# Optimization experiments

Hardware: AMD Instinct MI355X
Metric: run time of the kernel (lower is better)

Reference implementation:

```python
import jax, jax.numpy as jnp
import numpy as np

B, S, T = 32, 128, 64
V, E, H = 32000, 256, 512


def setup_inputs() -> dict:
    key = jax.random.key(0)
    ks = jax.random.split(key, 32)
    n = jax.random.normal

    def lin(k, fi, fo):
        kw, kb = jax.random.split(k)
        s = 1.0 / np.sqrt(fi)
        return (jax.random.uniform(kw, (fi, fo), jnp.float32, -s, s),
                jax.random.uniform(kb, (fo,), jnp.float32, -s, s))

    W_enc, b_enc = lin(ks[4], 2 * H, H)      # attention.enc_h_in
    W_prev, b_prev = lin(ks[5], H, H)        # attention.prev_s_in
    W_att, b_att = lin(ks[6], H, 1)          # attention.linear
    Wi_g, bi_g = lin(ks[7], E, 2 * H)        # cell.input_weights
    Wh_g, bh_g = lin(ks[8], H, 2 * H)        # cell.hidden_weights
    Wc_g, bc_g = lin(ks[9], 2 * H, 2 * H)    # cell.ctx_weights
    Wi, bi = lin(ks[10], E, H)               # cell.input_in
    Wh, bh = lin(ks[11], H, H)               # cell.hidden_in
    Wc, bc = lin(ks[12], 2 * H, H)           # cell.ctx_in
    W_out, b_out = lin(ks[13], H, V)         # dec2word

    return dict(
        content=n(ks[0], (B, H), jnp.float32),
        sentiment=n(ks[1], (B, H), jnp.float32),
        hiddens=n(ks[2], (B, S, 2 * H), jnp.float32),
        target=jax.random.randint(ks[3], (B, T), 0, V, jnp.int32),
        embed=n(ks[14], (V, E), jnp.float32) * 0.02,
        W_enc=W_enc, b_enc=b_enc, W_prev=W_prev, b_prev=b_prev,
        W_att=W_att, b_att=b_att,
        Wi_g=Wi_g, bi_g=bi_g, Wh_g=Wh_g, bh_g=bh_g, Wc_g=Wc_g, bc_g=bc_g,
        Wi=Wi, bi=bi, Wh=Wh, bh=bh, Wc=Wc, bc=bc,
        W_out=W_out, b_out=b_out,
    )


def reference(content, sentiment, hiddens, target, embed,
              W_enc, b_enc, W_prev, b_prev, W_att, b_att,
              Wi_g, bi_g, Wh_g, bh_g, Wc_g, bc_g,
              Wi, bi, Wh, bh, Wc, bc, W_out, b_out):
    tgt_emb = embed[target]                       # [B, T, E]
    enc_proj = hiddens @ W_enc + b_enc            # [B, S, H], timestep-invariant

    def step(prev_s, x_t):
        # additive attention
        q = prev_s @ W_prev + b_prev              # [B, H]
        h = jnp.tanh(enc_proj + q[:, None, :])    # [B, S, H]
        score = h @ W_att + b_att                 # [B, S, 1]
        alpha = jax.nn.softmax(score, axis=1)     # over source positions
        ctx = jnp.einsum('bsi,bsh->bh', alpha, hiddens)  # [B, 2H]
        # GRU-like cell (original uses only the first gate, as written)
        gates = x_t @ Wi_g + bi_g + prev_s @ Wh_g + bh_g + ctx @ Wc_g + bc_g
        reset_gate, _update_gate = jnp.split(gates, 2, axis=1)
        r = jax.nn.sigmoid(reset_gate)
        s_tilde = jnp.tanh(x_t @ Wi + bi + prev_s @ Wh + bh + ctx @ Wc + bc)
        new_s = (1.0 - r) * prev_s + r * s_tilde
        return new_s, new_s

    _, dec_h = jax.lax.scan(step, content, jnp.swapaxes(tgt_emb, 0, 1))
    dec_h = jnp.swapaxes(dec_h, 0, 1)             # [B, T, H]
    style_logits = sentiment @ W_out + b_out      # [B, V], same every step
    outputs = (dec_h @ W_out + b_out) + 0.5 * style_logits[:, None, :]
    return outputs                                # [B, T, V]
```

## Files before the change

### kernel.cpp

```cpp
#include <hip/hip_runtime.h>
#include <hip/hip_bf16.h>
#include <math.h>

#define NB 32
#define NS 128
#define NT 64
#define NV 32000
#define NE 256
#define NH 512

typedef short s16x8 __attribute__((ext_vector_type(8)));
typedef float f32x4 __attribute__((ext_vector_type(4)));
typedef unsigned u32x4 __attribute__((ext_vector_type(4)));

__device__ __forceinline__ unsigned short f2bf(float x) {
    union { float f; unsigned u; } v; v.f = x;
    unsigned r = v.u + 0x7FFFu + ((v.u >> 16) & 1u);
    return (unsigned short)(r >> 16);
}
__device__ __forceinline__ float bf2f(short h) {
    union { unsigned u; float f; } x;
    x.u = ((unsigned)(unsigned short)h) << 16;
    return x.f;
}

__device__ __forceinline__ void bar_lgkm() {
    asm volatile("s_waitcnt lgkmcnt(0)" ::: "memory");
    __builtin_amdgcn_sched_barrier(0);
    __builtin_amdgcn_s_barrier();
    __builtin_amdgcn_sched_barrier(0);
}

__device__ __forceinline__ void st_pt(unsigned long long* p, unsigned pay, unsigned tag) {
    unsigned long long v = (unsigned long long)pay | ((unsigned long long)tag << 32);
    asm volatile("global_store_dwordx2 %0, %1, off sc0 sc1" :: "v"(p), "v"(v) : "memory");
}
__device__ __forceinline__ void st_coh32(unsigned* p, unsigned v) {
    asm volatile("global_store_dword %0, %1, off sc0 sc1" :: "v"(p), "v"(v) : "memory");
}
__device__ __forceinline__ unsigned ld_coh32(const unsigned* p) {
    unsigned v;
    asm volatile("global_load_dword %0, %1, off sc0 sc1\n\ts_waitcnt vmcnt(0)"
                 : "=v"(v) : "v"(p) : "memory");
    return v;
}
__device__ __forceinline__ u32x4 ld_coh_x4(const void* p) {
    u32x4 v;
    asm volatile("global_load_dwordx4 %0, %1, off sc0 sc1\n\ts_waitcnt vmcnt(0)"
                 : "=&v"(v) : "v"(p) : "memory");
    return v;
}
__device__ __forceinline__ void ld8_pt(const unsigned long long* b0, unsigned long long* v) {
    unsigned long long v0, v1, v2, v3, v4, v5, v6, v7;
    asm volatile(
        "global_load_dwordx2 %0, %8, off sc0 sc1\n\t"
        "global_load_dwordx2 %1, %9, off sc0 sc1\n\t"
        "global_load_dwordx2 %2, %10, off sc0 sc1\n\t"
        "global_load_dwordx2 %3, %11, off sc0 sc1\n\t"
        "global_load_dwordx2 %4, %12, off sc0 sc1\n\t"
        "global_load_dwordx2 %5, %13, off sc0 sc1\n\t"
        "global_load_dwordx2 %6, %14, off sc0 sc1\n\t"
        "global_load_dwordx2 %7, %15, off sc0 sc1\n\t"
        "s_waitcnt vmcnt(0)"
        : "=&v"(v0), "=&v"(v1), "=&v"(v2), "=&v"(v3),
          "=&v"(v4), "=&v"(v5), "=&v"(v6), "=&v"(v7)
        : "v"(b0), "v"(b0 + 1024), "v"(b0 + 2048), "v"(b0 + 3072),
          "v"(b0 + 4096), "v"(b0 + 5120), "v"(b0 + 6144), "v"(b0 + 7168)
        : "memory");
    v[0] = v0; v[1] = v1; v[2] = v2; v[3] = v3;
    v[4] = v4; v[5] = v5; v[6] = v6; v[7] = v7;
}
__device__ __forceinline__ void ld3_pt(const unsigned long long* p0,
                                       const unsigned long long* p1,
                                       const unsigned long long* p2,
                                       unsigned long long& a, unsigned long long& b,
                                       unsigned long long& c) {
    asm volatile(
        "global_load_dwordx2 %0, %3, off sc0 sc1\n\t"
        "global_load_dwordx2 %1, %4, off sc0 sc1\n\t"
        "global_load_dwordx2 %2, %5, off sc0 sc1\n\t"
        "s_waitcnt vmcnt(0)"
        : "=&v"(a), "=&v"(b), "=&v"(c)
        : "v"(p0), "v"(p1), "v"(p2)
        : "memory");
}

__global__ void build_wfrag_k(const float* __restrict__ Wp,
                              const float* __restrict__ Whg,
                              const float* __restrict__ Wh,
                              unsigned short* __restrict__ wfrag) {
    int blk = blockIdx.x;
    int lane = threadIdx.x;
    int ct = blk >> 4, kt = blk & 15;
    int c = ct * 16 + (lane & 15);
    int kb = kt * 32 + (lane >> 4) * 8;
    s16x8 v;
#pragma unroll
    for (int j = 0; j < 8; ++j) {
        int k = kb + j;
        float x;
        if (c < 512)       x = Wp[k * 512 + c];
        else if (c < 1024) x = Whg[k * 1024 + (c - 512)];
        else               x = Wh[k * 512 + (c - 1024)];
        v[j] = (short)f2bf(x);
    }
    ((s16x8*)wfrag)[blk * 64 + lane] = v;
}

template<int MODE>
__global__ __launch_bounds__(256, 2) void gemm_mfma(
    const float* __restrict__ Af, const unsigned short* __restrict__ Abf,
    const int* __restrict__ gidx,
    const float* __restrict__ B0, const float* __restrict__ B1, const float* __restrict__ B2,
    const float* __restrict__ e0, const float* __restrict__ e1, const float* __restrict__ e2,
    const float* __restrict__ e3, const float* __restrict__ e4, const float* __restrict__ e5,
    void* __restrict__ O0v, void* __restrict__ O1v, void* __restrict__ O2v)
{
    constexpr int M   = (MODE == 0) ? 4096 : 2048;
    constexpr int K   = (MODE == 0) ? 1024 : 256;
    constexpr int LDA = (MODE == 0) ? 1024 : 256;
    constexpr int MB  = M / 128;

    const int bm = blockIdx.x % MB, bn = blockIdx.x / MB;
    const int m0 = bm * 128, n0 = bn * 128;

    const float* Bp; int ldb, coff;
    if constexpr (MODE == 0) {
        int sub = n0 >> 9;
        Bp   = (sub == 0) ? B0 : (sub == 1) ? B1 : B2;
        ldb  = (sub == 1) ? 1024 : 512;
        coff = n0 & 511;
    } else {
        if (n0 < 512) { Bp = B0; ldb = 1024; coff = n0; }
        else          { Bp = B1; ldb = 512;  coff = n0 - 512; }
    }

    __shared__ unsigned short As[128 * 40];
    __shared__ unsigned short Bs[128 * 40];

    const int tid = threadIdx.x, lane = tid & 63, w = tid >> 6;
    const int wr = w >> 1, wc = w & 1;
    const int k0f = (lane >> 4) * 8;
    const int rsel = lane & 15;

    f32x4 acc[4][4];
#pragma unroll
    for (int i = 0; i < 4; ++i)
#pragma unroll
        for (int j = 0; j < 4; ++j) { f32x4 z = {0.f, 0.f, 0.f, 0.f}; acc[i][j] = z; }

    for (int kt = 0; kt < K / 32; ++kt) {
        const int k0 = kt * 32;
        __syncthreads();
#pragma unroll
        for (int i = 0; i < 16; ++i) {
            int idx = tid + i * 256;
            int r = idx >> 5, k = idx & 31;
            unsigned short v;
            if constexpr (MODE == 1) {
                int g = gidx[m0 + r];
                v = f2bf(Af[(size_t)g * 256 + k0 + k]);
            } else {
                v = f2bf(Af[(size_t)(m0 + r) * LDA + k0 + k]);
            }
            As[r * 40 + k] = v;
        }
#pragma unroll
        for (int i = 0; i < 16; ++i) {
            int idx = tid + i * 256;
            int k = idx >> 7, c = idx & 127;
            Bs[c * 40 + k] = f2bf(Bp[(size_t)(k0 + k) * ldb + coff + c]);
        }
        __syncthreads();

        s16x8 af[4], bf[4];
#pragma unroll
        for (int i = 0; i < 4; ++i)
            af[i] = *(const s16x8*)&As[(wr * 64 + i * 16 + rsel) * 40 + k0f];
#pragma unroll
        for (int j = 0; j < 4; ++j)
            bf[j] = *(const s16x8*)&Bs[(wc * 64 + j * 16 + rsel) * 40 + k0f];
#pragma unroll
        for (int i = 0; i < 4; ++i)
#pragma unroll
            for (int j = 0; j < 4; ++j)
                acc[i][j] = __builtin_amdgcn_mfma_f32_16x16x32_bf16(af[i], bf[j], acc[i][j], 0, 0, 0);
    }

    const int rg = (lane >> 4) * 4;
#pragma unroll
    for (int i = 0; i < 4; ++i)
#pragma unroll
        for (int j = 0; j < 4; ++j) {
            int row0 = m0 + wr * 64 + i * 16 + rg;
            int col  = n0 + wc * 64 + j * 16 + rsel;
            if constexpr (MODE == 0) {
                int sub = col >> 9;
                if (sub == 0) {
                    unsigned short* Ta = (unsigned short*)O0v;
#pragma unroll
                    for (int r = 0; r < 4; ++r)
                        Ta[(size_t)(row0 + r) * 512 + col] = f2bf(tanhf(acc[i][j][r] + e0[col]));
                } else {
                    int h = col & 511;
                    int bb = row0 >> 7, s0 = row0 & 127;
                    unsigned long long pk = 0;
#pragma unroll
                    for (int r = 0; r < 4; ++r)
                        pk |= (unsigned long long)f2bf(acc[i][j][r]) << (16 * r);
                    unsigned short* dstp = (sub == 1) ? (unsigned short*)O1v : (unsigned short*)O2v;
                    *(unsigned long long*)&dstp[(size_t)((bb * 512 + h) * 128 + s0)] = pk;
                }
            } else {
                float* Of = (float*)O0v;
                float bias;
                if (col < 512) bias = e0[col] + e1[col] + e2[col];
                else { int h = col - 512; bias = e3[h] + e4[h] + e5[h]; }
#pragma unroll
                for (int r = 0; r < 4; ++r)
                    Of[(size_t)(row0 + r) * 1024 + col] = acc[i][j][r] + bias;
            }
        }
}

__global__ __launch_bounds__(1024) void fused_scan_out(
    const float* __restrict__ content, const float* __restrict__ sentiment,
    const float* __restrict__ b_prev,  const float* __restrict__ W_att,
    const unsigned short* __restrict__ Ta_bf,
    const unsigned short* __restrict__ hWcg_t,
    const unsigned short* __restrict__ hWc_t,
    const float* __restrict__ xgxs, const unsigned short* __restrict__ wfrag,
    unsigned long long* __restrict__ Spl, unsigned long long* __restrict__ Upl,
    unsigned short* __restrict__ dh, unsigned* __restrict__ prog,
    const float* __restrict__ W_out, const float* __restrict__ b_out,
    float* __restrict__ out)
{
    __shared__ __attribute__((aligned(16))) char smem[90624];
    const int tid = threadIdx.x, lane = tid & 63, w = tid >> 6;

    if (blockIdx.x < NB) {
        const int b = blockIdx.x;
        unsigned short* W_lds = (unsigned short*)smem;
        unsigned short* S_lds = (unsigned short*)(smem + 49152);
        float* tq = (float*)(smem + 83456);
        float* sc = (float*)(smem + 85504);
        float* al = (float*)(smem + 86016);
        float* cg = (float*)(smem + 86528);
        float* cs = (float*)(smem + 88576);

        {
            const s16x8* src = (const s16x8*)wfrag + (size_t)b * (3 * 16 * 64);
            s16x8* dst = (s16x8*)W_lds;
            for (int i = tid; i < 3 * 16 * 64; i += 1024) dst[i] = src[i];
        }
        float s_reg = 0.f, senth = 0.f, bprev_h = 0.f;
        if (tid < 512) {
            s_reg   = content[b * 512 + tid];
            senth   = 0.5f * sentiment[b * 512 + tid];
            bprev_h = b_prev[tid];
        }
        float wv[8];
        {
            const f32x4* wa = (const f32x4*)&W_att[lane * 8];
            f32x4 a0 = wa[0], a1 = wa[1];
#pragma unroll
            for (int j = 0; j < 4; ++j) { wv[j] = a0[j]; wv[4 + j] = a1[j]; }
        }
        const int kbase = (lane >> 4) * 8;
        const int mat = tid >> 9, hh = tid & 511;
        const s16x8* Mp = (const s16x8*)((mat ? hWc_t : hWcg_t) + ((size_t)(b * 512 + hh)) * 128);

        if (tid < 512) {
            float nsn = __shfl_down(s_reg, 1, 64);
            if (!(lane & 1)) {
                unsigned pay = (unsigned)f2bf(s_reg) | ((unsigned)f2bf(nsn) << 16);
                st_pt(&Spl[b * 256 + (tid >> 1)], pay, 1u);
            }
        }

        for (int t = 0; t < 64; ++t) {
            const unsigned want = (unsigned)(t + 1);
            float xg_pre = 0.f, xs_pre = 0.f;
            if (tid < 512) {
                xg_pre = xgxs[((size_t)b * 64 + t) * 1024 + tid];
                xs_pre = xgxs[((size_t)b * 64 + t) * 1024 + 512 + tid];
            }

            {
                unsigned long long v[8];
                const unsigned long long* base = &Spl[tid];
                ld8_pt(base, v);
                for (;;) {
                    bool ok = true;
#pragma unroll
                    for (int ii = 0; ii < 8; ++ii) ok &= ((unsigned)(v[ii] >> 32) == want);
                    if (ok) break;
                    __builtin_amdgcn_s_sleep(1);
                    ld8_pt(base, v);
                }
#pragma unroll
                for (int ii = 0; ii < 8; ++ii) {
                    int idx = tid + ii * 1024;
                    int r = idx >> 8, c = (idx & 255) * 2;
                    *(unsigned*)&S_lds[r * 536 + c] = (unsigned)v[ii];
                }
            }
            bar_lgkm();

            if (w < 6) {
                const int mt = w & 1, ct = w >> 1;
                const int arow = mt * 16 + (lane & 15);
                f32x4 ae = {0.f, 0.f, 0.f, 0.f}, ao = {0.f, 0.f, 0.f, 0.f};
                const s16x8* wl = (const s16x8*)W_lds;
#pragma unroll
                for (int kt = 0; kt < 16; kt += 2) {
                    s16x8 a0 = *(const s16x8*)&S_lds[arow * 536 + kt * 32 + kbase];
                    s16x8 a1 = *(const s16x8*)&S_lds[arow * 536 + (kt + 1) * 32 + kbase];
                    ae = __builtin_amdgcn_mfma_f32_16x16x32_bf16(a0, wl[(ct * 16 + kt) * 64 + lane], ae, 0, 0, 0);
                    ao = __builtin_amdgcn_mfma_f32_16x16x32_bf16(a1, wl[(ct * 16 + kt + 1) * 64 + lane], ao, 0, 0, 0);
                }
                f32x4 a4 = ae + ao;
                const int cout = b * 48 + ct * 16 + (lane & 15);
                const int rbase = mt * 16 + (lane >> 4) * 4;
#pragma unroll
                for (int r = 0; r < 4; ++r)
                    st_pt(&Upl[(size_t)(rbase + r) * 1536 + cout], __float_as_uint(a4[r]), want);
            }

            float guv = 0.f, suv = 0.f;
            if (tid < 512) {
                unsigned long long u0, u1, u2;
                const unsigned long long* q0 = &Upl[b * 1536 + tid];
                const unsigned long long* q1 = &Upl[b * 1536 + 512 + tid];
                const unsigned long long* q2 = &Upl[b * 1536 + 1024 + tid];
                ld3_pt(q0, q1, q2, u0, u1, u2);
                while (((unsigned)(u0 >> 32) != want) | ((unsigned)(u1 >> 32) != want) |
                       ((unsigned)(u2 >> 32) != want)) {
                    __builtin_amdgcn_s_sleep(1);
                    ld3_pt(q0, q1, q2, u0, u1, u2);
                }
                float qv = __uint_as_float((unsigned)u0);
                guv = __uint_as_float((unsigned)u1);
                suv = __uint_as_float((unsigned)u2);
                tq[tid] = tanhf(qv + bprev_h);
            }
            bar_lgkm();

            {
                float tqv[8];
                const f32x4* tp = (const f32x4*)&tq[lane * 8];
                f32x4 t0 = tp[0], t1 = tp[1];
#pragma unroll
                for (int j = 0; j < 4; ++j) { tqv[j] = t0[j]; tqv[4 + j] = t1[j]; }
#pragma unroll
                for (int s8 = 0; s8 < 8; ++s8) {
                    int s = w * 8 + s8;
                    s16x8 tv = *(const s16x8*)&Ta_bf[((size_t)(b * 128 + s)) * 512 + lane * 8];
                    float a = 0.f;
#pragma unroll
                    for (int j = 0; j < 8; ++j) {
                        float ta = bf2f(tv[j]);
                        float num = ta + tqv[j];
                        float den = fmaf(ta, tqv[j], 1.0f);
                        a = fmaf(wv[j], num * __builtin_amdgcn_rcpf(den), a);
                    }
#pragma unroll
                    for (int off = 32; off; off >>= 1) a += __shfl_xor(a, off, 64);
                    if (lane == 0) sc[s] = a;
                }
            }
            bar_lgkm();
            if (w == 0) {
                float v0 = sc[lane], v1 = sc[lane + 64];
                float m = fmaxf(v0, v1);
#pragma unroll
                for (int off = 32; off; off >>= 1) m = fmaxf(m, __shfl_xor(m, off, 64));
                float p0 = __expf(v0 - m), p1 = __expf(v1 - m);
                float sm = p0 + p1;
#pragma unroll
                for (int off = 32; off; off >>= 1) sm += __shfl_xor(sm, off, 64);
                float inv = __builtin_amdgcn_rcpf(sm);
                al[lane] = p0 * inv; al[lane + 64] = p1 * inv;
            }
            bar_lgkm();
            {
                float a0 = 0.f, a1 = 0.f;
#pragma unroll
                for (int q = 0; q < 16; ++q) {
                    s16x8 v = Mp[q];
#pragma unroll
                    for (int j = 0; j < 8; j += 2) {
                        a0 = fmaf(al[q * 8 + j],     bf2f(v[j]),     a0);
                        a1 = fmaf(al[q * 8 + j + 1], bf2f(v[j + 1]), a1);
                    }
                }
                if (mat) cs[hh] = a0 + a1; else cg[hh] = a0 + a1;
            }
            bar_lgkm();
            if (tid < 512) {
                int h = tid;
                float g  = guv + xg_pre + cg[h];
                float r  = __builtin_amdgcn_rcpf(1.0f + __expf(-g));
                float sp = suv + xs_pre + cs[h];
                float e  = __expf(2.0f * sp);
                float st = 1.0f - 2.0f * __builtin_amdgcn_rcpf(e + 1.0f);
                float ns = s_reg + r * (st - s_reg);
                s_reg = ns;
                float dv = ns + senth;
                float dvn = __shfl_down(dv, 1, 64);
                if (!(lane & 1)) {
                    unsigned pk = (unsigned)f2bf(dv) | ((unsigned)f2bf(dvn) << 16);
                    st_coh32((unsigned*)dh + ((((size_t)t * 32 + b) * 512 + h) >> 1), pk);
                }
                if (t < 63) {
                    float nsn = __shfl_down(ns, 1, 64);
                    if (!(lane & 1)) {
                        unsigned pay = (unsigned)f2bf(ns) | ((unsigned)f2bf(nsn) << 16);
                        st_pt(&Spl[b * 256 + (h >> 1)], pay, (unsigned)(t + 2));
                    }
                }
            }
            if ((t & 7) == 7) asm volatile("s_waitcnt vmcnt(0)" ::: "memory");
            bar_lgkm();
            if ((t & 7) == 7 && tid == 0)
                st_coh32(&prog[b * 16], (unsigned)(t + 1));
        }
    } else {
        unsigned short* As = (unsigned short*)smem;
        unsigned short* Bs = (unsigned short*)(smem + 20480);
        const int k4 = blockIdx.x - NB;
        const int wr = w >> 2, wc = w & 3;
        const int k0f = (lane >> 4) * 8;
        const int rsel = lane & 15;
        const int rg = (lane >> 4) * 4;
        const int ar = tid >> 2, akofs = (tid & 3) * 8;
        const int bk = tid >> 5, bc8 = (tid & 31) * 8;

        for (int idx = k4; idx < 1000; idx += 224) {
            const int tm = idx / 125, tn = idx - tm * 125;
            const unsigned need = (unsigned)(tm * 8 + 8);
            if (w == 0) {
                for (;;) {
                    unsigned v = 0xFFFFFFFFu;
                    if (lane < 32) v = ld_coh32(&prog[lane * 16]);
                    if (__all(v >= need)) break;
                    __builtin_amdgcn_s_sleep(32);
                }
            }
            __syncthreads();

            const int m0 = tm * 256, n0 = tn * 256;
            f32x4 acc[4][4];
#pragma unroll
            for (int i = 0; i < 4; ++i)
#pragma unroll
                for (int j = 0; j < 4; ++j) { f32x4 z = {0.f, 0.f, 0.f, 0.f}; acc[i][j] = z; }

            for (int kt = 0; kt < 16; ++kt) {
                const int k0 = kt * 32;
                __syncthreads();
                {
                    u32x4 a = ld_coh_x4(&dh[(size_t)(m0 + ar) * 512 + k0 + akofs]);
                    *(u32x4*)&As[ar * 40 + akofs] = a;
                }
                {
                    const float* bp = &W_out[(size_t)(k0 + bk) * 32000 + n0 + bc8];
#pragma unroll
                    for (int j = 0; j < 8; ++j) Bs[(bc8 + j) * 40 + bk] = f2bf(bp[j]);
                }
                __syncthreads();

                s16x8 af[4], bfr[4];
#pragma unroll
                for (int i = 0; i < 4; ++i)
                    af[i] = *(const s16x8*)&As[(wr * 64 + i * 16 + rsel) * 40 + k0f];
#pragma unroll
                for (int j = 0; j < 4; ++j)
                    bfr[j] = *(const s16x8*)&Bs[(wc * 64 + j * 16 + rsel) * 40 + k0f];
#pragma unroll
                for (int i = 0; i < 4; ++i)
#pragma unroll
                    for (int j = 0; j < 4; ++j)
                        acc[i][j] = __builtin_amdgcn_mfma_f32_16x16x32_bf16(af[i], bfr[j], acc[i][j], 0, 0, 0);
            }

#pragma unroll
            for (int i = 0; i < 4; ++i)
#pragma unroll
                for (int j = 0; j < 4; ++j) {
                    int trow0 = m0 + wr * 64 + i * 16 + rg;
                    int col   = n0 + wc * 64 + j * 16 + rsel;
                    float bb_ = 1.5f * b_out[col];
#pragma unroll
                    for (int r = 0; r < 4; ++r) {
                        int trow = trow0 + r;
                        int bb = trow & 31, tt = trow >> 5;
                        out[(size_t)(bb * 64 + tt) * 32000 + col] = acc[i][j][r] + bb_;
                    }
                }
        }
    }
}

extern "C" void kernel_launch(void* const* d_in, const int* in_sizes, int n_in,
                              void* d_out, int out_size, void* d_ws, size_t ws_size,
                              hipStream_t stream) {
    const float* content  = (const float*)d_in[0];
    const float* sentiment= (const float*)d_in[1];
    const float* hiddens  = (const float*)d_in[2];
    const int*   target   = (const int*)  d_in[3];
    const float* embed    = (const float*)d_in[4];
    const float* W_enc = (const float*)d_in[5];  const float* b_enc = (const float*)d_in[6];
    const float* W_prev= (const float*)d_in[7];  const float* b_prev= (const float*)d_in[8];
    const float* W_att = (const float*)d_in[9];
    const float* Wi_g  = (const float*)d_in[11]; const float* bi_g  = (const float*)d_in[12];
    const float* Wh_g  = (const float*)d_in[13]; const float* bh_g  = (const float*)d_in[14];
    const float* Wc_g  = (const float*)d_in[15]; const float* bc_g  = (const float*)d_in[16];
    const float* Wi    = (const float*)d_in[17]; const float* bi    = (const float*)d_in[18];
    const float* Wh    = (const float*)d_in[19]; const float* bh    = (const float*)d_in[20];
    const float* Wc    = (const float*)d_in[21]; const float* bc    = (const float*)d_in[22];
    const float* W_out = (const float*)d_in[23]; const float* b_out = (const float*)d_in[24];
    float* out = (float*)d_out;

    char* ws = (char*)d_ws;
    unsigned short* wfrag = (unsigned short*)ws;
    unsigned long long* Spl = (unsigned long long*)(ws + 0x180000);
    unsigned long long* Upl = (unsigned long long*)(ws + 0x190000);
    unsigned* prog = (unsigned*)(ws + 0x1F0000);
    unsigned short* Ta_bf   = (unsigned short*)(ws + 0x200000);
    unsigned short* hWcg_t  = (unsigned short*)(ws + 0x600000);
    unsigned short* hWc_t   = (unsigned short*)(ws + 0xA00000);
    float* xgxs     = (float*)(ws + 0xE00000);
    unsigned short* dh      = (unsigned short*)(ws + 0x1600000);

    hipMemsetAsync(ws + 0x180000, 0, 0x70800, stream);

    build_wfrag_k<<<96 * 16, 64, 0, stream>>>(W_prev, Wh_g, Wh, wfrag);

    gemm_mfma<0><<<32 * 12, 256, 0, stream>>>(
        hiddens, nullptr, nullptr, W_enc, Wc_g, Wc,
        b_enc, nullptr, nullptr, nullptr, nullptr, nullptr,
        (void*)Ta_bf, (void*)hWcg_t, (void*)hWc_t);

    gemm_mfma<1><<<16 * 8, 256, 0, stream>>>(
        embed, nullptr, target, Wi_g, Wi, nullptr,
        bi_g, bh_g, bc_g, bi, bh, bc,
        (void*)xgxs, nullptr, nullptr);

    fused_scan_out<<<256, 1024, 0, stream>>>(
        content, sentiment, b_prev, W_att, Ta_bf, hWcg_t, hWc_t,
        xgxs, wfrag, Spl, Upl, dh, prog, W_out, b_out, out);

    (void)in_sizes; (void)n_in; (void)out_size; (void)ws_size;
}
```

Measured before the change: 1.337 ms.

## Prepack W_out into MFMA-fragment bf16 layout before output GEMM

```diff
diff --git a/kernel.cpp b/kernel.cpp
--- a/kernel.cpp
+++ b/kernel.cpp
@@ -44,11 +44,18 @@
                  : "=v"(v) : "v"(p) : "memory");
     return v;
 }
-__device__ __forceinline__ u32x4 ld_coh_x4(const void* p) {
-    u32x4 v;
-    asm volatile("global_load_dwordx4 %0, %1, off sc0 sc1\n\ts_waitcnt vmcnt(0)"
-                 : "=&v"(v) : "v"(p) : "memory");
-    return v;
+__device__ __forceinline__ void st_coh_x4(void* p, u32x4 v) {
+    asm volatile("global_store_dwordx4 %0, %1, off sc0 sc1" :: "v"(p), "v"(v) : "memory");
+}
+__device__ __forceinline__ void ld64_coh(const void* p, u32x4& a, u32x4& b, u32x4& c, u32x4& d) {
+    asm volatile(
+        "global_load_dwordx4 %0, %4, off sc0 sc1\n\t"
+        "global_load_dwordx4 %1, %4, off offset:16 sc0 sc1\n\t"
+        "global_load_dwordx4 %2, %4, off offset:32 sc0 sc1\n\t"
+        "global_load_dwordx4 %3, %4, off offset:48 sc0 sc1\n\t"
+        "s_waitcnt vmcnt(0)"
+        : "=&v"(a), "=&v"(b), "=&v"(c), "=&v"(d)
+        : "v"(p) : "memory");
 }
 __device__ __forceinline__ void ld8_pt(const unsigned long long* b0, unsigned long long* v) {
     unsigned long long v0, v1, v2, v3, v4, v5, v6, v7;
@@ -232,6 +239,7 @@
     const float* __restrict__ xgxs, const unsigned short* __restrict__ wfrag,
     unsigned long long* __restrict__ Spl, unsigned long long* __restrict__ Upl,
     unsigned short* __restrict__ dh, unsigned* __restrict__ prog,
+    unsigned* __restrict__ packdone, unsigned short* __restrict__ wpk,
     const float* __restrict__ W_out, const float* __restrict__ b_out,
     float* __restrict__ out)
 {
@@ -426,15 +434,38 @@
                 st_coh32(&prog[b * 16], (unsigned)(t + 1));
         }
     } else {
+        const int k4 = blockIdx.x - NB;
         unsigned short* As = (unsigned short*)smem;
-        unsigned short* Bs = (unsigned short*)(smem + 20480);
-        const int k4 = blockIdx.x - NB;
+
+        for (int u = k4 * 16 + w; u < 32000; u += 224 * 16) {
+            int ct = u >> 4, kt = u & 15;
+            int c = ct * 16 + (lane & 15);
+            int kb = kt * 32 + (lane >> 4) * 8;
+            s16x8 v;
+#pragma unroll
+            for (int j = 0; j < 8; ++j)
+                v[j] = (short)f2bf(W_out[(size_t)(kb + j) * 32000 + c]);
+            union { s16x8 s; u32x4 u4; } cv; cv.s = v;
+            st_coh_x4(&wpk[(size_t)u * 512 + (size_t)lane * 8], cv.u4);
+        }
+        asm volatile("s_waitcnt vmcnt(0)" ::: "memory");
+        __syncthreads();
+        if (tid == 0)
+            __hip_atomic_fetch_add(packdone, 1u, __ATOMIC_RELAXED, __HIP_MEMORY_SCOPE_AGENT);
+        if (w == 0 && lane == 0) {
+            while (__hip_atomic_load(packdone, __ATOMIC_RELAXED, __HIP_MEMORY_SCOPE_AGENT) < 224u)
+                __builtin_amdgcn_s_sleep(16);
+        }
+        __syncthreads();
+        __builtin_amdgcn_fence(__ATOMIC_ACQUIRE, "agent");
+        __syncthreads();
+
         const int wr = w >> 2, wc = w & 3;
         const int k0f = (lane >> 4) * 8;
         const int rsel = lane & 15;
         const int rg = (lane >> 4) * 4;
-        const int ar = tid >> 2, akofs = (tid & 3) * 8;
-        const int bk = tid >> 5, bc8 = (tid & 31) * 8;
+        const int ar4 = tid >> 2, aq = tid & 3;
+        const s16x8* wpk8 = (const s16x8*)wpk;
 
         for (int idx = k4; idx < 1000; idx += 224) {
             const int tm = idx / 125, tn = idx - tm * 125;
@@ -456,32 +487,36 @@
 #pragma unroll
                 for (int j = 0; j < 4; ++j) { f32x4 z = {0.f, 0.f, 0.f, 0.f}; acc[i][j] = z; }
 
-            for (int kt = 0; kt < 16; ++kt) {
-                const int k0 = kt * 32;
+#pragma unroll
+            for (int kq = 0; kq < 4; ++kq) {
                 __syncthreads();
                 {
-                    u32x4 a = ld_coh_x4(&dh[(size_t)(m0 + ar) * 512 + k0 + akofs]);
-                    *(u32x4*)&As[ar * 40 + akofs] = a;
-                }
-                {
-                    const float* bp = &W_out[(size_t)(k0 + bk) * 32000 + n0 + bc8];
-#pragma unroll
-                    for (int j = 0; j < 8; ++j) Bs[(bc8 + j) * 40 + bk] = f2bf(bp[j]);
+                    const unsigned short* sp = &dh[(size_t)(m0 + ar4) * 512 + kq * 128 + aq * 32];
+                    u32x4 a0, a1, a2, a3;
+                    ld64_coh(sp, a0, a1, a2, a3);
+                    int base = ar4 * 136 + aq * 32;
+                    *(u32x4*)&As[base]      = a0;
+                    *(u32x4*)&As[base + 8]  = a1;
+                    *(u32x4*)&As[base + 16] = a2;
+                    *(u32x4*)&As[base + 24] = a3;
                 }
                 __syncthreads();
-
-                s16x8 af[4], bfr[4];
-#pragma unroll
-                for (int i = 0; i < 4; ++i)
-                    af[i] = *(const s16x8*)&As[(wr * 64 + i * 16 + rsel) * 40 + k0f];
-#pragma unroll
-                for (int j = 0; j < 4; ++j)
-                    bfr[j] = *(const s16x8*)&Bs[(wc * 64 + j * 16 + rsel) * 40 + k0f];
-#pragma unroll
-                for (int i = 0; i < 4; ++i)
+#pragma unroll
+                for (int kk = 0; kk < 4; ++kk) {
+                    const int kt = kq * 4 + kk;
+                    s16x8 bfr[4], af[4];
 #pragma unroll
                     for (int j = 0; j < 4; ++j)
-                        acc[i][j] = __builtin_amdgcn_mfma_f32_16x16x32_bf16(af[i], bfr[j], acc[i][j], 0, 0, 0);
+                        bfr[j] = wpk8[(size_t)(((tn * 16 + wc * 4 + j) * 16 + kt)) * 64 + lane];
+#pragma unroll
+                    for (int i = 0; i < 4; ++i)
+                        af[i] = *(const s16x8*)&As[(wr * 64 + i * 16 + rsel) * 136 + kk * 32 + k0f];
+#pragma unroll
+                    for (int i = 0; i < 4; ++i)
+#pragma unroll
+                        for (int j = 0; j < 4; ++j)
+                            acc[i][j] = __builtin_amdgcn_mfma_f32_16x16x32_bf16(af[i], bfr[j], acc[i][j], 0, 0, 0);
+                }
             }
 
 #pragma unroll
@@ -527,13 +562,15 @@
     unsigned long long* Spl = (unsigned long long*)(ws + 0x180000);
     unsigned long long* Upl = (unsigned long long*)(ws + 0x190000);
     unsigned* prog = (unsigned*)(ws + 0x1F0000);
+    unsigned* packdone = (unsigned*)(ws + 0x1F0800);
     unsigned short* Ta_bf   = (unsigned short*)(ws + 0x200000);
     unsigned short* hWcg_t  = (unsigned short*)(ws + 0x600000);
     unsigned short* hWc_t   = (unsigned short*)(ws + 0xA00000);
     float* xgxs     = (float*)(ws + 0xE00000);
     unsigned short* dh      = (unsigned short*)(ws + 0x1600000);
-
-    hipMemsetAsync(ws + 0x180000, 0, 0x70800, stream);
+    unsigned short* wpk     = (unsigned short*)(ws + 0x1800000);
+
+    hipMemsetAsync(ws + 0x180000, 0, 0x71000, stream);
 
     build_wfrag_k<<<96 * 16, 64, 0, stream>>>(W_prev, Wh_g, Wh, wfrag);
 
@@ -549,7 +586,7 @@
 
     fused_scan_out<<<256, 1024, 0, stream>>>(
         content, sentiment, b_prev, W_att, Ta_bf, hWcg_t, hWc_t,
-        xgxs, wfrag, Spl, Upl, dh, prog, W_out, b_out, out);
+        xgxs, wfrag, Spl, Upl, dh, prog, packdone, wpk, W_out, b_out, out);
 
     (void)in_sizes; (void)n_in; (void)out_size; (void)ws_size;
 }
```

Measured after the change: 1.283 ms. -4.0%, faster.
